# Kernel tuning notes

Measured on AMD Instinct MI355X. Metric: run time of the kernel, lower is better.

Reference implementation:

```python
import jax, jax.numpy as jnp
import numpy as np

TOP_K = 2  # init arg top_k
EPS = 1e-9


def setup_inputs() -> dict:
    key = jax.random.key(0)
    ks = jax.random.split(key, 5)
    B, L, D, E, H, G = 2, 2048, 2048, 8, 2048, 256
    s = lambda k, sh, fan: jax.random.normal(k, sh, jnp.float32) / np.sqrt(fan)
    return {
        "x": jax.random.normal(ks[0], (B, L, D), jnp.float32),
        "wg1": s(ks[1], (D, G), D),
        "wg2": s(ks[2], (G, E), G),
        "w1": s(ks[3], (E, D, H), D),
        "w2": s(ks[4], (E, H, D), H),
    }


def reference(x, wg1, wg2, w1, w2):
    B, L, D = x.shape
    xf = x.reshape(-1, D)                                  # [T, D]
    T = xf.shape[0]

    # --- top-k gating (mlp gate) ---
    logits = jax.nn.gelu(xf @ wg1) @ wg2                   # [T, E]
    probs = jax.nn.softmax(logits, axis=-1)                # [T, E]
    top_vals, top_idx = jax.lax.top_k(probs, TOP_K)        # [T, k]
    # dense gate matrix: gate weight where expert selected, else 0
    gates = jnp.zeros_like(probs).at[jnp.arange(T)[:, None], top_idx].set(top_vals)  # [T, E]

    # --- grouped expert FFN (dense-equivalent of gather/grouped-GEMM/scatter) ---
    h = jax.nn.gelu(jnp.einsum('td,edh->teh', xf, w1))     # [T, E, H]
    gh = h * gates[:, :, None]                             # fold gates in (linear in h)
    y = jnp.einsum('teh,ehd->td', gh, w2).reshape(B, L, D)

    # --- mutual-information aux loss: -H(E) + H(E|X) ---
    p_mean = probs.mean(axis=0)                            # [E]
    loss = jnp.sum(p_mean * jnp.log(p_mean + EPS)) \
         - jnp.mean(jnp.sum(probs * jnp.log(probs + EPS), axis=-1))
    return y, loss
```

## Files before the change

kernel.cpp:

```cpp
#include <hip/hip_runtime.h>

#define T_TOK 4096
#define NROWS_MAX 10240
#define MAX_TILES 40

typedef float  fv4  __attribute__((ext_vector_type(4)));
typedef __bf16 bv4  __attribute__((ext_vector_type(4)));
typedef __bf16 bv8  __attribute__((ext_vector_type(8)));

#define CTRL_OFF     0
#define ROWTOK_OFF   4096
#define ROWGATE_OFF  45056
#define TOPIDX_OFF   86016
#define TOPVAL_OFF   118784
#define G_OFF        151552
#define XB_OFF       4345856
#define W1T_OFF      21123072
#define W2T_OFF      88231936
#define HBUF_OFF     155340800

struct Ctrl {
    int   counts[8];
    float psum[8];
    float entsum;
    int   ntiles;
    int   off[8];
    int   tile_e[MAX_TILES];
    int   tile_r0[MAX_TILES];
};

__device__ __forceinline__ float gelu_f(float x) {
    float x3 = x * x * x;
    return 0.5f * x * (1.0f + tanhf(0.7978845608028654f * (x + 0.044715f * x3)));
}

__device__ __forceinline__ void g2l16(const void* gptr, void* lptr) {
    __builtin_amdgcn_global_load_lds(
        (const __attribute__((address_space(1))) void*)gptr,
        (__attribute__((address_space(3))) void*)lptr, 16, 0, 0);
}

__global__ __launch_bounds__(256) void transpose_cvt(
    const float* __restrict__ w1, const float* __restrict__ w2,
    __bf16* __restrict__ w1t, __bf16* __restrict__ w2t)
{
    int b    = blockIdx.x;
    int mat  = b >> 10;
    int tile = b & 1023;
    int trow = tile >> 5, tcol = tile & 31;
    const float* src = (mat < 8) ? (w1 + (size_t)mat * 4194304)
                                 : (w2 + (size_t)(mat - 8) * 4194304);
    __bf16* dst = (mat < 8) ? (w1t + (size_t)mat * 4194304)
                            : (w2t + (size_t)(mat - 8) * 4194304);
    __shared__ float tileS[64][65];
    int tid = threadIdx.x;
    int c = tid & 63, r4 = tid >> 6;
#pragma unroll
    for (int u = 0; u < 16; u++) {
        int rr = u * 4 + r4;
        tileS[rr][c] = src[(size_t)(trow * 64 + rr) * 2048 + tcol * 64 + c];
    }
    __syncthreads();
    int c2 = (tid & 31) * 2, r8 = tid >> 5;
#pragma unroll
    for (int u = 0; u < 8; u++) {
        int rr = u * 8 + r8;
        __bf16 v0 = (__bf16)tileS[c2][rr];
        __bf16 v1 = (__bf16)tileS[c2 + 1][rr];
        size_t o = (size_t)(tcol * 64 + rr) * 2048 + trow * 64 + c2;
        dst[o]     = v0;
        dst[o + 1] = v1;
    }
}

__global__ __launch_bounds__(256) void cvt_x_kernel(const float* __restrict__ x,
                                                    __bf16* __restrict__ xb)
{
    size_t idx = ((size_t)blockIdx.x * 256 + threadIdx.x) * 4;
    fv4 v = *(const fv4*)(x + idx);
    bv4 o;
#pragma unroll
    for (int u = 0; u < 4; u++) o[u] = (__bf16)v[u];
    *(bv4*)(xb + idx) = o;
}

__global__ __launch_bounds__(256) void gating_gemm(const float* __restrict__ x,
                                                   const float* __restrict__ wg1,
                                                   float* __restrict__ g)
{
    __shared__ float As[16][68];
    __shared__ float Bs[16][68];
    int tid = threadIdx.x;
    int tx = tid & 15, ty = tid >> 4;
    int mb = blockIdx.x, nb = blockIdx.y;
    float acc[4][4];
#pragma unroll
    for (int u = 0; u < 4; u++)
#pragma unroll
        for (int v = 0; v < 4; v++) acc[u][v] = 0.f;

    int r  = tid >> 2, kq = tid & 3;
    int kb = tid >> 4, n4 = (tid & 15) * 4;
    const float* gx = x + (size_t)(mb * 64 + r) * 2048 + kq * 4;
    const float* gw = wg1 + nb * 64 + n4;

    for (int k0 = 0; k0 < 2048; k0 += 16) {
        fv4 av = *(const fv4*)(gx + k0);
        fv4 bv = *(const fv4*)(gw + (size_t)(k0 + kb) * 256);
        __syncthreads();
#pragma unroll
        for (int u = 0; u < 4; u++) As[kq * 4 + u][r] = av[u];
        *(fv4*)&Bs[kb][n4] = bv;
        __syncthreads();
#pragma unroll
        for (int k = 0; k < 16; k++) {
            fv4 a = *(const fv4*)&As[k][ty * 4];
            fv4 b = *(const fv4*)&Bs[k][tx * 4];
#pragma unroll
            for (int u = 0; u < 4; u++)
#pragma unroll
                for (int v = 0; v < 4; v++) acc[u][v] += a[u] * b[v];
        }
    }
#pragma unroll
    for (int u = 0; u < 4; u++) {
        int row = mb * 64 + ty * 4 + u;
#pragma unroll
        for (int v = 0; v < 4; v++)
            g[(size_t)row * 256 + nb * 64 + tx * 4 + v] = gelu_f(acc[u][v]);
    }
}

__global__ __launch_bounds__(256) void gate_kernel(
    const float* __restrict__ g, const float* __restrict__ wg2,
    Ctrl* __restrict__ ctrl, int* __restrict__ topidx, float* __restrict__ topval)
{
    __shared__ float wg2s[256 * 9];
    __shared__ float psum_s[8];
    __shared__ float ent_s;
    __shared__ int   cnt_s[8];
    int tid = threadIdx.x;
    for (int i = tid; i < 2048; i += 256) {
        int k = i >> 3, e = i & 7;
        wg2s[k * 9 + e] = wg2[i];
    }
    if (tid < 8) { psum_s[tid] = 0.f; cnt_s[tid] = 0; }
    if (tid == 8) ent_s = 0.f;
    __syncthreads();

    int lane = tid & 63, wv = tid >> 6;
    int t = blockIdx.x * 4 + wv;
    fv4 g4 = *(const fv4*)&g[(size_t)t * 256 + lane * 4];
    float part[8];
#pragma unroll
    for (int e = 0; e < 8; e++) part[e] = 0.f;
#pragma unroll
    for (int u = 0; u < 4; u++) {
        int k = lane * 4 + u;
        float gv = g4[u];
#pragma unroll
        for (int e = 0; e < 8; e++) part[e] += gv * wg2s[k * 9 + e];
    }
#pragma unroll
    for (int e = 0; e < 8; e++)
        for (int off = 32; off; off >>= 1) part[e] += __shfl_xor(part[e], off);

    if (lane == 0) {
        float mx = part[0];
#pragma unroll
        for (int e = 1; e < 8; e++) mx = fmaxf(mx, part[e]);
        float p[8], Z = 0.f;
#pragma unroll
        for (int e = 0; e < 8; e++) { p[e] = expf(part[e] - mx); Z += p[e]; }
        float rz = 1.f / Z;
#pragma unroll
        for (int e = 0; e < 8; e++) p[e] *= rz;
        int i0 = 0;
#pragma unroll
        for (int e = 1; e < 8; e++) if (part[e] > part[i0]) i0 = e;
        int i1 = (i0 == 0) ? 1 : 0;
#pragma unroll
        for (int e = 0; e < 8; e++)
            if (e != i0 && part[e] > part[i1]) i1 = e;
        topidx[2 * t]     = i0;
        topidx[2 * t + 1] = i1;
        topval[2 * t]     = p[i0];
        topval[2 * t + 1] = p[i1];
        float ent = 0.f;
#pragma unroll
        for (int e = 0; e < 8; e++) ent += p[e] * logf(p[e] + 1e-9f);
#pragma unroll
        for (int e = 0; e < 8; e++) atomicAdd(&psum_s[e], p[e]);
        atomicAdd(&ent_s, ent);
        atomicAdd(&cnt_s[i0], 1);
        atomicAdd(&cnt_s[i1], 1);
    }
    __syncthreads();
    if (tid < 8)                    atomicAdd(&ctrl->psum[tid], psum_s[tid]);
    else if (tid == 8)              atomicAdd(&ctrl->entsum, ent_s);
    else if (tid >= 16 && tid < 24) atomicAdd(&ctrl->counts[tid - 16], cnt_s[tid - 16]);
}

__global__ __launch_bounds__(256) void route_kernel(
    Ctrl* __restrict__ ctrl, const int* __restrict__ topidx,
    const float* __restrict__ topval, int* __restrict__ rowtok,
    float* __restrict__ rowgate)
{
    __shared__ int cur[8];
    __shared__ int offs_s[8];
    int tid = threadIdx.x;
    if (tid == 0) {
        int off = 0, nt = 0;
        for (int e = 0; e < 8; e++) {
            offs_s[e]    = off;
            ctrl->off[e] = off;
            int c = ctrl->counts[e];
            for (int m = 0; m < c; m += 256) {
                ctrl->tile_e[nt]  = e;
                ctrl->tile_r0[nt] = off + m;
                nt++;
            }
            off += ((c + 255) >> 8) << 8;
        }
        ctrl->ntiles = nt;
    }
    if (tid < 8) cur[tid] = 0;
    __syncthreads();
    for (int t = tid; t < T_TOK; t += 256) {
#pragma unroll
        for (int k = 0; k < 2; k++) {
            int e = topidx[2 * t + k];
            int p = atomicAdd(&cur[e], 1);
            int row = offs_s[e] + p;
            rowtok[row]  = t;
            rowgate[row] = topval[2 * t + k];
        }
    }
}

#define WAIT_VM4 0x0F74
#define WAIT_VM0 0x0F70
template <bool IS_FFN1>
__global__ __launch_bounds__(512, 2) void gemm_grouped(
    const __bf16* __restrict__ A,
    const __bf16* __restrict__ Bt,
    const Ctrl* __restrict__ ctrl,
    const int* __restrict__ rowtok,
    const float* __restrict__ rowgate,
    __bf16* __restrict__ hbuf,
    float* __restrict__ y)
{
    const int K = 2048;
    __shared__ __bf16 smem[3 * 16384];

    int tid  = threadIdx.x;
    int lane = tid & 63, w = tid >> 6;
    int wr = w >> 1, wc = w & 1;
    int c0 = 2 * w, c1 = c0 + 1;
    int sub = lane >> 2;
    int kcg = (lane & 3) ^ ((lane >> 3) & 3);
    int frow = (lane & 15) * 32 + (((lane >> 4) ^ ((lane >> 1) & 3)) * 8);

    int ntiles = ctrl->ntiles;
    int x = blockIdx.x & 7, s = blockIdx.x >> 3;

    int items[2]; int ni = 0;
    {
        int i0 = x * 32 + s;
        int tl = ((i0 >> 5) << 2) | (i0 & 3);
        if (tl < ntiles) items[ni++] = i0;
    }
    if (s < 8) {
        int i1 = 256 + x * 8 + s;
        int tl = ((i1 >> 5) << 2) | (i1 & 3);
        if (tl < ntiles) items[ni++] = i1;
    }

    for (int it = 0; it < ni; it++) {
        int item = items[it];
        int idx  = item & 31;
        int tl   = ((item >> 5) << 2) | (idx & 3);
        int nb   = (idx >> 2) & 7;
        int e    = ctrl->tile_e[tl];
        int r0   = ctrl->tile_r0[tl];

        size_t ga0, ga1;
        if constexpr (IS_FFN1) {
            ga0 = (size_t)rowtok[r0 + c0 * 16 + sub] * K;
            ga1 = (size_t)rowtok[r0 + c1 * 16 + sub] * K;
        } else {
            ga0 = (size_t)(r0 + c0 * 16 + sub) * K;
            ga1 = (size_t)(r0 + c1 * 16 + sub) * K;
        }
        const __bf16* pA0 = A + ga0 + kcg * 8;
        const __bf16* pA1 = A + ga1 + kcg * 8;
        const __bf16* pB0 = Bt + ((size_t)e * 2048 + nb * 256 + c0 * 16 + sub) * K + kcg * 8;
        const __bf16* pB1 = Bt + ((size_t)e * 2048 + nb * 256 + c1 * 16 + sub) * K + kcg * 8;

        fv4 acc[4][8];
#pragma unroll
        for (int i = 0; i < 4; i++)
#pragma unroll
            for (int j = 0; j < 8; j++) acc[i][j] = (fv4)0.0f;

        __builtin_amdgcn_s_barrier();
#pragma unroll
        for (int pk = 0; pk < 2; pk++) {
            __bf16* lb = smem + pk * 16384;
            g2l16(pA0 + pk * 32, lb + c0 * 512);
            g2l16(pA1 + pk * 32, lb + c1 * 512);
            g2l16(pB0 + pk * 32, lb + 8192 + c0 * 512);
            g2l16(pB1 + pk * 32, lb + 8192 + c1 * 512);
        }

        int bcur = 0;
        for (int k = 0; k < 64; k++) {
            if (k < 63) __builtin_amdgcn_s_waitcnt(WAIT_VM4);
            else        __builtin_amdgcn_s_waitcnt(WAIT_VM0);
            __builtin_amdgcn_s_barrier();
            if (k < 62) {
                int bnext = bcur + 32768; if (bnext >= 49152) bnext -= 49152;
                __bf16* lb = smem + bnext;
                int ke = (k + 2) * 32;
                g2l16(pA0 + ke, lb + c0 * 512);
                g2l16(pA1 + ke, lb + c1 * 512);
                g2l16(pB0 + ke, lb + 8192 + c0 * 512);
                g2l16(pB1 + ke, lb + 8192 + c1 * 512);
            }
            const __bf16* lb = smem + bcur;
            bv8 aF[4], bF[8];
#pragma unroll
            for (int i = 0; i < 4; i++)
                aF[i] = *(const bv8*)&lb[(wr * 64 + i * 16) * 32 + frow];
#pragma unroll
            for (int j = 0; j < 8; j++)
                bF[j] = *(const bv8*)&lb[8192 + (wc * 128 + j * 16) * 32 + frow];
#pragma unroll
            for (int i = 0; i < 4; i++)
#pragma unroll
                for (int j = 0; j < 8; j++)
                    acc[i][j] = __builtin_amdgcn_mfma_f32_16x16x32_bf16(aF[i], bF[j], acc[i][j], 0, 0, 0);
            bcur += 16384; if (bcur >= 49152) bcur -= 49152;
        }

        int colb = nb * 256 + wc * 128 + (lane & 15);
        int rb   = r0 + wr * 64 + (lane >> 4) * 4;
#pragma unroll
        for (int i = 0; i < 4; i++) {
#pragma unroll
            for (int rr = 0; rr < 4; rr++) {
                int rg = rb + i * 16 + rr;
                if constexpr (IS_FFN1) {
                    float gate = rowgate[rg];
                    size_t ho = (size_t)rg * 2048;
#pragma unroll
                    for (int j = 0; j < 8; j++)
                        hbuf[ho + colb + j * 16] = (__bf16)(gelu_f(acc[i][j][rr]) * gate);
                } else {
                    size_t yo = (size_t)rowtok[rg] * 2048;
#pragma unroll
                    for (int j = 0; j < 8; j++)
                        atomicAdd(&y[yo + colb + j * 16], acc[i][j][rr]);
                }
            }
        }
    }
}

__global__ __launch_bounds__(64) void loss_kernel(const Ctrl* __restrict__ ctrl,
                                                  float* __restrict__ out)
{
    if (threadIdx.x == 0) {
        float a = 0.f;
#pragma unroll
        for (int e = 0; e < 8; e++) {
            float pm = ctrl->psum[e] * (1.0f / 4096.0f);
            a += pm * logf(pm + 1e-9f);
        }
        out[0] = a - ctrl->entsum * (1.0f / 4096.0f);
    }
}

extern "C" void kernel_launch(void* const* d_in, const int* in_sizes, int n_in,
                              void* d_out, int out_size, void* d_ws, size_t ws_size,
                              hipStream_t stream)
{
    const float* x   = (const float*)d_in[0];
    const float* wg1 = (const float*)d_in[1];
    const float* wg2 = (const float*)d_in[2];
    const float* w1  = (const float*)d_in[3];
    const float* w2  = (const float*)d_in[4];
    float* out = (float*)d_out;

    char* ws = (char*)d_ws;
    Ctrl*   ctrl    = (Ctrl*)(ws + CTRL_OFF);
    int*    rowtok  = (int*)(ws + ROWTOK_OFF);
    float*  rowgate = (float*)(ws + ROWGATE_OFF);
    int*    topidx  = (int*)(ws + TOPIDX_OFF);
    float*  topval  = (float*)(ws + TOPVAL_OFF);
    float*  g       = (float*)(ws + G_OFF);
    __bf16* xb      = (__bf16*)(ws + XB_OFF);
    __bf16* w1t     = (__bf16*)(ws + W1T_OFF);
    __bf16* w2t     = (__bf16*)(ws + W2T_OFF);
    __bf16* hbuf    = (__bf16*)(ws + HBUF_OFF);

    hipMemsetAsync(ws + CTRL_OFF, 0, 4096, stream);
    hipMemsetAsync(ws + ROWTOK_OFF, 0, 81920, stream);
    hipMemsetAsync(d_out, 0, (size_t)out_size * sizeof(float), stream);

    transpose_cvt<<<16384, 256, 0, stream>>>(w1, w2, w1t, w2t);
    cvt_x_kernel<<<8192, 256, 0, stream>>>(x, xb);
    gating_gemm<<<dim3(64, 4), 256, 0, stream>>>(x, wg1, g);
    gate_kernel<<<1024, 256, 0, stream>>>(g, wg2, ctrl, topidx, topval);
    route_kernel<<<1, 256, 0, stream>>>(ctrl, topidx, topval, rowtok, rowgate);
    gemm_grouped<true><<<256, 512, 0, stream>>>(xb, w1t, ctrl, rowtok, rowgate, hbuf, nullptr);
    gemm_grouped<false><<<256, 512, 0, stream>>>(hbuf, w2t, ctrl, rowtok, rowgate, nullptr, out);
    loss_kernel<<<1, 64, 0, stream>>>(ctrl, out + 8388608);
}
```

Baseline: 874.1 us.

## Restructure grouped GEMM main loop into quadrant-split ping-pong with BK=64

Rewrites the grouped expert GEMM inner loop to use a K-tile of 64 with double-buffered 64KB shared memory, split into four 128x128 quadrant sub-steps. Each sub-step interleaves global-to-LDS loads with MFMA bursts separated by barriers and raises wave priority around the MFMAs. The wave layout changes from 4x2 to 2x4 with a new XOR swizzle. This is meant to overlap memory traffic with matrix math more finely and cut per-iteration barrier overhead. In exchange it adds more barriers per K-step, larger LDS use that may limit occupancy, and a more complex schedule.

```diff
diff --git a/kernel.cpp b/kernel.cpp
--- a/kernel.cpp
+++ b/kernel.cpp
@@ -240,6 +240,65 @@
 
 #define WAIT_VM4 0x0F74
 #define WAIT_VM0 0x0F70
+
+__device__ __forceinline__ void ld_af8(const __bf16* sm, int off, int l15, int pb8,
+                                       bv8 f[4][2]) {
+#pragma unroll
+    for (int mi = 0; mi < 4; mi++)
+#pragma unroll
+        for (int ks = 0; ks < 2; ks++)
+            f[mi][ks] = *(const bv8*)&sm[off + mi * 1024 + l15 * 64 + (pb8 ^ (ks << 5))];
+}
+
+__device__ __forceinline__ void ld_bf4(const __bf16* sm, int off, int l15, int pb8,
+                                       bv8 f[2][2]) {
+#pragma unroll
+    for (int ni = 0; ni < 2; ni++)
+#pragma unroll
+        for (int ks = 0; ks < 2; ks++)
+            f[ni][ks] = *(const bv8*)&sm[off + ni * 1024 + l15 * 64 + (pb8 ^ (ks << 5))];
+}
+
+__device__ __forceinline__ void mm16(fv4 ac[4][2], const bv8 a[4][2], const bv8 b[2][2]) {
+    __builtin_amdgcn_s_setprio(1);
+#pragma unroll
+    for (int mi = 0; mi < 4; mi++)
+#pragma unroll
+        for (int ni = 0; ni < 2; ni++)
+#pragma unroll
+            for (int ks = 0; ks < 2; ks++)
+                ac[mi][ni] = __builtin_amdgcn_mfma_f32_16x16x32_bf16(
+                    a[mi][ks], b[ni][ks], ac[mi][ni], 0, 0, 0);
+    __builtin_amdgcn_s_setprio(0);
+}
+
+#define VM4 __builtin_amdgcn_s_waitcnt(WAIT_VM4)
+#define VM0 __builtin_amdgcn_s_waitcnt(WAIT_VM0)
+#define BAR __builtin_amdgcn_s_barrier()
+
+#define KT_STEP(BUF, KN)                                                          \
+    {                                                                             \
+        const int Ab = (BUF) * 16384, Bb = 32768 + (BUF) * 16384;                 \
+        const int An = ((BUF) ^ 1) * 16384, Bn = 32768 + (((BUF) ^ 1) * 16384);   \
+        bv8 aF[4][2], bF0[2][2], bF1[2][2];                                       \
+        ld_af8(smem, Ab + A0W, l15, pb8, aF);                                     \
+        ld_bf4(smem, Bb + B0W, l15, pb8, bF0);                                    \
+        g2l16(pa00 + (KN), smem + An + stbase);                                   \
+        g2l16(pa01 + (KN), smem + An + 4096 + stbase);                            \
+        VM4; BAR; mm16(acc[0][0], aF, bF0); BAR;                                  \
+        ld_bf4(smem, Bb + B1W, l15, pb8, bF1);                                    \
+        g2l16(pb00 + (KN), smem + Bn + stbase);                                   \
+        g2l16(pb01 + (KN), smem + Bn + 4096 + stbase);                            \
+        VM4; BAR; mm16(acc[0][1], aF, bF1); BAR;                                  \
+        ld_af8(smem, Ab + A1W, l15, pb8, aF);                                     \
+        g2l16(pb10 + (KN), smem + Bn + 8192 + stbase);                            \
+        g2l16(pb11 + (KN), smem + Bn + 8192 + 4096 + stbase);                     \
+        VM4; BAR; mm16(acc[1][1], aF, bF1); BAR;                                  \
+        g2l16(pa10 + (KN), smem + An + 8192 + stbase);                            \
+        g2l16(pa11 + (KN), smem + An + 8192 + 4096 + stbase);                     \
+        VM4; BAR; mm16(acc[1][0], aF, bF0); BAR;                                  \
+    }
+
 template <bool IS_FFN1>
 __global__ __launch_bounds__(512, 2) void gemm_grouped(
     const __bf16* __restrict__ A,
@@ -250,16 +309,23 @@
     __bf16* __restrict__ hbuf,
     float* __restrict__ y)
 {
-    const int K = 2048;
-    __shared__ __bf16 smem[3 * 16384];
-
-    int tid  = threadIdx.x;
-    int lane = tid & 63, w = tid >> 6;
-    int wr = w >> 1, wc = w & 1;
-    int c0 = 2 * w, c1 = c0 + 1;
-    int sub = lane >> 2;
-    int kcg = (lane & 3) ^ ((lane >> 3) & 3);
-    int frow = (lane & 15) * 32 + (((lane >> 4) ^ ((lane >> 1) & 3)) * 8);
+    __shared__ __bf16 smem[65536];
+
+    const int tid  = threadIdx.x;
+    const int lane = tid & 63, w = tid >> 6;
+    const int wm = w >> 2, wn = w & 3;
+    const int l15 = lane & 15;
+    const int pb8 = (((lane >> 4) ^ (lane & 7)) << 3);
+    const int rowL = (lane >> 4) * 4;
+
+    const int A0W = wm * 4096;
+    const int A1W = 8192 + wm * 4096;
+    const int B0W = wn * 2048;
+    const int B1W = 8192 + wn * 2048;
+
+    const int srow   = tid >> 3;
+    const int schunk = (tid & 7) ^ ((tid >> 3) & 7);
+    const int stbase = w * 512;
 
     int ntiles = ctrl->ntiles;
     int x = blockIdx.x & 7, s = blockIdx.x >> 3;
@@ -284,83 +350,101 @@
         int e    = ctrl->tile_e[tl];
         int r0   = ctrl->tile_r0[tl];
 
-        size_t ga0, ga1;
+        size_t ar00, ar01, ar10, ar11;
         if constexpr (IS_FFN1) {
-            ga0 = (size_t)rowtok[r0 + c0 * 16 + sub] * K;
-            ga1 = (size_t)rowtok[r0 + c1 * 16 + sub] * K;
+            ar00 = (size_t)rowtok[r0 + srow];
+            ar01 = (size_t)rowtok[r0 + 64 + srow];
+            ar10 = (size_t)rowtok[r0 + 128 + srow];
+            ar11 = (size_t)rowtok[r0 + 192 + srow];
         } else {
-            ga0 = (size_t)(r0 + c0 * 16 + sub) * K;
-            ga1 = (size_t)(r0 + c1 * 16 + sub) * K;
-        }
-        const __bf16* pA0 = A + ga0 + kcg * 8;
-        const __bf16* pA1 = A + ga1 + kcg * 8;
-        const __bf16* pB0 = Bt + ((size_t)e * 2048 + nb * 256 + c0 * 16 + sub) * K + kcg * 8;
-        const __bf16* pB1 = Bt + ((size_t)e * 2048 + nb * 256 + c1 * 16 + sub) * K + kcg * 8;
-
-        fv4 acc[4][8];
-#pragma unroll
-        for (int i = 0; i < 4; i++)
-#pragma unroll
-            for (int j = 0; j < 8; j++) acc[i][j] = (fv4)0.0f;
-
-        __builtin_amdgcn_s_barrier();
-#pragma unroll
-        for (int pk = 0; pk < 2; pk++) {
-            __bf16* lb = smem + pk * 16384;
-            g2l16(pA0 + pk * 32, lb + c0 * 512);
-            g2l16(pA1 + pk * 32, lb + c1 * 512);
-            g2l16(pB0 + pk * 32, lb + 8192 + c0 * 512);
-            g2l16(pB1 + pk * 32, lb + 8192 + c1 * 512);
-        }
-
-        int bcur = 0;
-        for (int k = 0; k < 64; k++) {
-            if (k < 63) __builtin_amdgcn_s_waitcnt(WAIT_VM4);
-            else        __builtin_amdgcn_s_waitcnt(WAIT_VM0);
-            __builtin_amdgcn_s_barrier();
-            if (k < 62) {
-                int bnext = bcur + 32768; if (bnext >= 49152) bnext -= 49152;
-                __bf16* lb = smem + bnext;
-                int ke = (k + 2) * 32;
-                g2l16(pA0 + ke, lb + c0 * 512);
-                g2l16(pA1 + ke, lb + c1 * 512);
-                g2l16(pB0 + ke, lb + 8192 + c0 * 512);
-                g2l16(pB1 + ke, lb + 8192 + c1 * 512);
-            }
-            const __bf16* lb = smem + bcur;
-            bv8 aF[4], bF[8];
-#pragma unroll
-            for (int i = 0; i < 4; i++)
-                aF[i] = *(const bv8*)&lb[(wr * 64 + i * 16) * 32 + frow];
-#pragma unroll
-            for (int j = 0; j < 8; j++)
-                bF[j] = *(const bv8*)&lb[8192 + (wc * 128 + j * 16) * 32 + frow];
-#pragma unroll
-            for (int i = 0; i < 4; i++)
-#pragma unroll
-                for (int j = 0; j < 8; j++)
-                    acc[i][j] = __builtin_amdgcn_mfma_f32_16x16x32_bf16(aF[i], bF[j], acc[i][j], 0, 0, 0);
-            bcur += 16384; if (bcur >= 49152) bcur -= 49152;
-        }
-
-        int colb = nb * 256 + wc * 128 + (lane & 15);
-        int rb   = r0 + wr * 64 + (lane >> 4) * 4;
-#pragma unroll
-        for (int i = 0; i < 4; i++) {
-#pragma unroll
-            for (int rr = 0; rr < 4; rr++) {
-                int rg = rb + i * 16 + rr;
-                if constexpr (IS_FFN1) {
-                    float gate = rowgate[rg];
-                    size_t ho = (size_t)rg * 2048;
-#pragma unroll
-                    for (int j = 0; j < 8; j++)
-                        hbuf[ho + colb + j * 16] = (__bf16)(gelu_f(acc[i][j][rr]) * gate);
-                } else {
-                    size_t yo = (size_t)rowtok[rg] * 2048;
-#pragma unroll
-                    for (int j = 0; j < 8; j++)
-                        atomicAdd(&y[yo + colb + j * 16], acc[i][j][rr]);
+            ar00 = (size_t)(r0 + srow);
+            ar01 = (size_t)(r0 + 64 + srow);
+            ar10 = (size_t)(r0 + 128 + srow);
+            ar11 = (size_t)(r0 + 192 + srow);
+        }
+        const __bf16* pa00 = A + ar00 * 2048 + schunk * 8;
+        const __bf16* pa01 = A + ar01 * 2048 + schunk * 8;
+        const __bf16* pa10 = A + ar10 * 2048 + schunk * 8;
+        const __bf16* pa11 = A + ar11 * 2048 + schunk * 8;
+        size_t bb = (size_t)e * 2048 + nb * 256;
+        const __bf16* pb00 = Bt + (bb + srow) * 2048 + schunk * 8;
+        const __bf16* pb01 = Bt + (bb + 64 + srow) * 2048 + schunk * 8;
+        const __bf16* pb10 = Bt + (bb + 128 + srow) * 2048 + schunk * 8;
+        const __bf16* pb11 = Bt + (bb + 192 + srow) * 2048 + schunk * 8;
+
+        fv4 acc[2][2][4][2];
+#pragma unroll
+        for (int qa = 0; qa < 2; qa++)
+#pragma unroll
+            for (int qb = 0; qb < 2; qb++)
+#pragma unroll
+                for (int mi = 0; mi < 4; mi++)
+#pragma unroll
+                    for (int nj = 0; nj < 2; nj++) acc[qa][qb][mi][nj] = (fv4)0.0f;
+
+        BAR;
+        g2l16(pa00, smem + stbase);
+        g2l16(pa01, smem + 4096 + stbase);
+        g2l16(pb00, smem + 32768 + stbase);
+        g2l16(pb01, smem + 32768 + 4096 + stbase);
+        g2l16(pb10, smem + 32768 + 8192 + stbase);
+        g2l16(pb11, smem + 32768 + 8192 + 4096 + stbase);
+        g2l16(pa10, smem + 8192 + stbase);
+        g2l16(pa11, smem + 8192 + 4096 + stbase);
+        VM4;
+        BAR;
+
+#pragma unroll 1
+        for (int k2 = 0; k2 < 15; k2++) {
+            int kn = ((k2 * 2) + 1) << 6;
+            KT_STEP(0, kn);
+            KT_STEP(1, kn + 64);
+        }
+        KT_STEP(0, 31 << 6);
+
+        {
+            bv8 aF[4][2], bF0[2][2], bF1[2][2];
+            ld_af8(smem, 16384 + A0W, l15, pb8, aF);
+            ld_bf4(smem, 49152 + B0W, l15, pb8, bF0);
+            VM0;
+            BAR;
+            mm16(acc[0][0], aF, bF0);
+            ld_bf4(smem, 49152 + B1W, l15, pb8, bF1);
+            mm16(acc[0][1], aF, bF1);
+            ld_af8(smem, 16384 + A1W, l15, pb8, aF);
+            mm16(acc[1][1], aF, bF1);
+            mm16(acc[1][0], aF, bF0);
+        }
+
+#pragma unroll
+        for (int qa = 0; qa < 2; qa++) {
+#pragma unroll
+            for (int mi = 0; mi < 4; mi++) {
+                int rbase = r0 + qa * 128 + wm * 64 + mi * 16 + rowL;
+#pragma unroll
+                for (int rr = 0; rr < 4; rr++) {
+                    int rg = rbase + rr;
+                    if constexpr (IS_FFN1) {
+                        float gate = rowgate[rg];
+                        size_t ho = (size_t)rg * 2048;
+#pragma unroll
+                        for (int qb = 0; qb < 2; qb++)
+#pragma unroll
+                            for (int nj = 0; nj < 2; nj++) {
+                                int col = nb * 256 + qb * 128 + wn * 32 + nj * 16 + l15;
+                                hbuf[ho + col] =
+                                    (__bf16)(gelu_f(acc[qa][qb][mi][nj][rr]) * gate);
+                            }
+                    } else {
+                        size_t yo = (size_t)rowtok[rg] * 2048;
+#pragma unroll
+                        for (int qb = 0; qb < 2; qb++)
+#pragma unroll
+                            for (int nj = 0; nj < 2; nj++) {
+                                int col = nb * 256 + qb * 128 + wn * 32 + nj * 16 + l15;
+                                atomicAdd(&y[yo + col], acc[qa][qb][mi][nj][rr]);
+                            }
+                    }
                 }
             }
         }
```

New measurement: 886.7 us. No clear change (+1.4%).

## Shrink grouped GEMM tiles to 128x128 with grid-stride scheduling over more blocks

Applied to the files above, without the earlier changes.

Replaces the 256x256-tile, 512-thread, triple-buffered async-pipelined grouped GEMM with a 128x128-tile, 256-thread kernel. It uses a single LDS buffer with two barriers per K step, and a grid-stride loop over 768 blocks. Expert row padding drops from 256 to 128, which cuts wasted rows and improves load balance across CUs. In exchange it loses the prefetch pipelining and the swizzled LDS layout, which can add bank conflicts. Each loaded tile is also reused less, so global and LDS traffic per FLOP rises.

```diff
diff --git a/kernel.cpp b/kernel.cpp
--- a/kernel.cpp
+++ b/kernel.cpp
@@ -2,7 +2,7 @@
 
 #define T_TOK 4096
 #define NROWS_MAX 10240
-#define MAX_TILES 40
+#define MAX_TILES 72
 
 typedef float  fv4  __attribute__((ext_vector_type(4)));
 typedef __bf16 bv4  __attribute__((ext_vector_type(4)));
@@ -215,12 +215,12 @@
             offs_s[e]    = off;
             ctrl->off[e] = off;
             int c = ctrl->counts[e];
-            for (int m = 0; m < c; m += 256) {
+            for (int m = 0; m < c; m += 128) {
                 ctrl->tile_e[nt]  = e;
                 ctrl->tile_r0[nt] = off + m;
                 nt++;
             }
-            off += ((c + 255) >> 8) << 8;
+            off += ((c + 127) >> 7) << 7;
         }
         ctrl->ntiles = nt;
     }
@@ -238,10 +238,10 @@
     }
 }
 
-#define WAIT_VM4 0x0F74
-#define WAIT_VM0 0x0F70
+#define NBLK 768
+
 template <bool IS_FFN1>
-__global__ __launch_bounds__(512, 2) void gemm_grouped(
+__global__ __launch_bounds__(256, 3) void gemm_grouped(
     const __bf16* __restrict__ A,
     const __bf16* __restrict__ Bt,
     const Ctrl* __restrict__ ctrl,
@@ -250,101 +250,71 @@
     __bf16* __restrict__ hbuf,
     float* __restrict__ y)
 {
-    const int K = 2048;
-    __shared__ __bf16 smem[3 * 16384];
-
-    int tid  = threadIdx.x;
-    int lane = tid & 63, w = tid >> 6;
-    int wr = w >> 1, wc = w & 1;
-    int c0 = 2 * w, c1 = c0 + 1;
-    int sub = lane >> 2;
-    int kcg = (lane & 3) ^ ((lane >> 3) & 3);
-    int frow = (lane & 15) * 32 + (((lane >> 4) ^ ((lane >> 1) & 3)) * 8);
+    __shared__ __bf16 As[128 * 32];
+    __shared__ __bf16 Bs[128 * 32];
+
+    const int tid  = threadIdx.x;
+    const int lane = tid & 63, w = tid >> 6;
+    const int wm = w >> 1, wn = w & 1;
+    const int l15 = lane & 15;
+    const int kq8 = (lane >> 4) * 8;
+    const int stb = w * 512;
+    const int srow = tid >> 2;
+    const int sk8  = (tid & 3) * 8;
 
     int ntiles = ctrl->ntiles;
-    int x = blockIdx.x & 7, s = blockIdx.x >> 3;
-
-    int items[2]; int ni = 0;
-    {
-        int i0 = x * 32 + s;
-        int tl = ((i0 >> 5) << 2) | (i0 & 3);
-        if (tl < ntiles) items[ni++] = i0;
-    }
-    if (s < 8) {
-        int i1 = 256 + x * 8 + s;
-        int tl = ((i1 >> 5) << 2) | (i1 & 3);
-        if (tl < ntiles) items[ni++] = i1;
-    }
-
-    for (int it = 0; it < ni; it++) {
-        int item = items[it];
-        int idx  = item & 31;
-        int tl   = ((item >> 5) << 2) | (idx & 3);
-        int nb   = (idx >> 2) & 7;
-        int e    = ctrl->tile_e[tl];
-        int r0   = ctrl->tile_r0[tl];
-
-        size_t ga0, ga1;
+    int nitems = ntiles << 4;
+    int sw = (blockIdx.x & 7) * (NBLK / 8) + (blockIdx.x >> 3);
+
+    for (int item = sw; item < nitems; item += NBLK) {
+        int tl = item >> 4, nb = item & 15;
+        int e  = ctrl->tile_e[tl];
+        int r0 = ctrl->tile_r0[tl];
+
+        int rA0, rA1;
         if constexpr (IS_FFN1) {
-            ga0 = (size_t)rowtok[r0 + c0 * 16 + sub] * K;
-            ga1 = (size_t)rowtok[r0 + c1 * 16 + sub] * K;
+            rA0 = rowtok[r0 + srow];
+            rA1 = rowtok[r0 + 64 + srow];
         } else {
-            ga0 = (size_t)(r0 + c0 * 16 + sub) * K;
-            ga1 = (size_t)(r0 + c1 * 16 + sub) * K;
-        }
-        const __bf16* pA0 = A + ga0 + kcg * 8;
-        const __bf16* pA1 = A + ga1 + kcg * 8;
-        const __bf16* pB0 = Bt + ((size_t)e * 2048 + nb * 256 + c0 * 16 + sub) * K + kcg * 8;
-        const __bf16* pB1 = Bt + ((size_t)e * 2048 + nb * 256 + c1 * 16 + sub) * K + kcg * 8;
-
-        fv4 acc[4][8];
+            rA0 = r0 + srow;
+            rA1 = rA0 + 64;
+        }
+        const __bf16* pa0 = A + (size_t)rA0 * 2048 + sk8;
+        const __bf16* pa1 = A + (size_t)rA1 * 2048 + sk8;
+        const __bf16* pb0 = Bt + ((size_t)e * 2048 + nb * 128 + srow) * 2048 + sk8;
+        const __bf16* pb1 = pb0 + (size_t)64 * 2048;
+
+        fv4 acc[4][4];
 #pragma unroll
         for (int i = 0; i < 4; i++)
 #pragma unroll
-            for (int j = 0; j < 8; j++) acc[i][j] = (fv4)0.0f;
-
-        __builtin_amdgcn_s_barrier();
-#pragma unroll
-        for (int pk = 0; pk < 2; pk++) {
-            __bf16* lb = smem + pk * 16384;
-            g2l16(pA0 + pk * 32, lb + c0 * 512);
-            g2l16(pA1 + pk * 32, lb + c1 * 512);
-            g2l16(pB0 + pk * 32, lb + 8192 + c0 * 512);
-            g2l16(pB1 + pk * 32, lb + 8192 + c1 * 512);
-        }
-
-        int bcur = 0;
-        for (int k = 0; k < 64; k++) {
-            if (k < 63) __builtin_amdgcn_s_waitcnt(WAIT_VM4);
-            else        __builtin_amdgcn_s_waitcnt(WAIT_VM0);
-            __builtin_amdgcn_s_barrier();
-            if (k < 62) {
-                int bnext = bcur + 32768; if (bnext >= 49152) bnext -= 49152;
-                __bf16* lb = smem + bnext;
-                int ke = (k + 2) * 32;
-                g2l16(pA0 + ke, lb + c0 * 512);
-                g2l16(pA1 + ke, lb + c1 * 512);
-                g2l16(pB0 + ke, lb + 8192 + c0 * 512);
-                g2l16(pB1 + ke, lb + 8192 + c1 * 512);
-            }
-            const __bf16* lb = smem + bcur;
-            bv8 aF[4], bF[8];
+            for (int j = 0; j < 4; j++) acc[i][j] = (fv4)0.0f;
+
+        for (int k = 0; k < 2048; k += 32) {
+            __syncthreads();
+            g2l16(pa0 + k, As + stb);
+            g2l16(pa1 + k, As + 2048 + stb);
+            g2l16(pb0 + k, Bs + stb);
+            g2l16(pb1 + k, Bs + 2048 + stb);
+            __syncthreads();
+
+            bv8 aF[4], bF[4];
 #pragma unroll
             for (int i = 0; i < 4; i++)
-                aF[i] = *(const bv8*)&lb[(wr * 64 + i * 16) * 32 + frow];
-#pragma unroll
-            for (int j = 0; j < 8; j++)
-                bF[j] = *(const bv8*)&lb[8192 + (wc * 128 + j * 16) * 32 + frow];
+                aF[i] = *(const bv8*)&As[(wm * 64 + i * 16 + l15) * 32 + kq8];
+#pragma unroll
+            for (int j = 0; j < 4; j++)
+                bF[j] = *(const bv8*)&Bs[(wn * 64 + j * 16 + l15) * 32 + kq8];
 #pragma unroll
             for (int i = 0; i < 4; i++)
 #pragma unroll
-                for (int j = 0; j < 8; j++)
-                    acc[i][j] = __builtin_amdgcn_mfma_f32_16x16x32_bf16(aF[i], bF[j], acc[i][j], 0, 0, 0);
-            bcur += 16384; if (bcur >= 49152) bcur -= 49152;
-        }
-
-        int colb = nb * 256 + wc * 128 + (lane & 15);
-        int rb   = r0 + wr * 64 + (lane >> 4) * 4;
+                for (int j = 0; j < 4; j++)
+                    acc[i][j] = __builtin_amdgcn_mfma_f32_16x16x32_bf16(
+                        aF[i], bF[j], acc[i][j], 0, 0, 0);
+        }
+
+        int colb = nb * 128 + wn * 64 + l15;
+        int rb   = r0 + wm * 64 + (lane >> 4) * 4;
 #pragma unroll
         for (int i = 0; i < 4; i++) {
 #pragma unroll
@@ -354,12 +324,12 @@
                     float gate = rowgate[rg];
                     size_t ho = (size_t)rg * 2048;
 #pragma unroll
-                    for (int j = 0; j < 8; j++)
+                    for (int j = 0; j < 4; j++)
                         hbuf[ho + colb + j * 16] = (__bf16)(gelu_f(acc[i][j][rr]) * gate);
                 } else {
                     size_t yo = (size_t)rowtok[rg] * 2048;
 #pragma unroll
-                    for (int j = 0; j < 8; j++)
+                    for (int j = 0; j < 4; j++)
                         atomicAdd(&y[yo + colb + j * 16], acc[i][j][rr]);
                 }
             }
@@ -413,7 +383,7 @@
     gating_gemm<<<dim3(64, 4), 256, 0, stream>>>(x, wg1, g);
     gate_kernel<<<1024, 256, 0, stream>>>(g, wg2, ctrl, topidx, topval);
     route_kernel<<<1, 256, 0, stream>>>(ctrl, topidx, topval, rowtok, rowgate);
-    gemm_grouped<true><<<256, 512, 0, stream>>>(xb, w1t, ctrl, rowtok, rowgate, hbuf, nullptr);
-    gemm_grouped<false><<<256, 512, 0, stream>>>(hbuf, w2t, ctrl, rowtok, rowgate, nullptr, out);
+    gemm_grouped<true><<<NBLK, 256, 0, stream>>>(xb, w1t, ctrl, rowtok, rowgate, hbuf, nullptr);
+    gemm_grouped<false><<<NBLK, 256, 0, stream>>>(hbuf, w2t, ctrl, rowtok, rowgate, nullptr, out);
     loss_kernel<<<1, 64, 0, stream>>>(ctrl, out + 8388608);
 }
```

New measurement: 832.3 us. -4.8%, faster.
